# Performance work log

Measured on AMD Instinct MI355X. Metric: run time of the kernel, lower is better.

The kernel has to match this reference:

```python
import jax, jax.numpy as jnp
import numpy as np

B, L, C, H = 4, 2048, 1024, 16
D = C // H
MAX_SCALE_MUL = float(np.log(100.0))
EPS = 1e-12


def setup_inputs() -> dict:
    key = jax.random.key(0)
    ks = jax.random.split(key, 7)
    return {
        "x": jax.random.normal(ks[0], (B, L, C), dtype=jnp.float32),
        "W_qkv": jax.random.normal(ks[1], (3 * C, C), dtype=jnp.float32) * (C ** -0.5),
        "q_bias": jax.random.normal(ks[2], (C,), dtype=jnp.float32) * 0.02,
        "v_bias": jax.random.normal(ks[3], (C,), dtype=jnp.float32) * 0.02,
        "scale_mul_log": jnp.full((1, H, 1, 1), np.log(4.0), dtype=jnp.float32),
        "W_proj": jax.random.normal(ks[4], (C, C), dtype=jnp.float32) * (C ** -0.5),
        "b_proj": jax.random.normal(ks[5], (C,), dtype=jnp.float32) * 0.02,
    }


def reference(x, W_qkv, q_bias, v_bias, scale_mul_log, W_proj, b_proj):
    Bb, Ll, Cc = x.shape
    # fused QKV projection with bias = cat(q_bias, zeros, v_bias)
    bias = jnp.concatenate([q_bias, jnp.zeros_like(q_bias), v_bias])
    qkv = (x @ W_qkv.T + bias).reshape(Bb, Ll, 3, H, D)
    q, k, v = (jnp.transpose(qkv[:, :, i], (0, 2, 1, 3)) for i in range(3))  # [B,H,L,D]
    # L2-norm attention: normalize q,k; learned per-head scale on q (clamped)
    scale_mul = jnp.exp(jnp.minimum(scale_mul_log, MAX_SCALE_MUL))  # [1,H,1,1]
    q = q / jnp.maximum(jnp.linalg.norm(q, axis=-1, keepdims=True), EPS) * scale_mul
    k = k / jnp.maximum(jnp.linalg.norm(k, axis=-1, keepdims=True), EPS)
    # SDPA with scale=1 (attn_l2_norm path), no mask, no dropout (eval)
    scores = jnp.einsum("bhqd,bhkd->bhqk", q, k)
    attn = jax.nn.softmax(scores, axis=-1)
    out = jnp.einsum("bhqk,bhkd->bhqd", attn, v)
    out = jnp.transpose(out, (0, 2, 1, 3)).reshape(Bb, Ll, Cc)
    return out @ W_proj.T + b_proj
```

## Files before the change

kernel.cpp:

```cpp
#include <hip/hip_runtime.h>
#include <hip/hip_bf16.h>


typedef __attribute__((ext_vector_type(8))) short bf16x8;
typedef __attribute__((ext_vector_type(4))) float f32x4;
typedef __attribute__((ext_vector_type(16))) float f32x16;

#define MAXLOG 4.60517018598809f
#define LOG2E  1.4426950408889634f

__device__ __forceinline__ float bf2f(unsigned short u) {
    union { unsigned int i; float f; } v; v.i = ((unsigned int)u) << 16; return v.f;
}
__device__ __forceinline__ unsigned short f2bf(float f) {
    union { float f; unsigned int i; } v; v.f = f;
    unsigned int x = v.i;
    return (unsigned short)((x + 0x7FFFu + ((x >> 16) & 1u)) >> 16);
}
__device__ __forceinline__ bf16x8 pack8(const float* __restrict__ p) {
    float4 a = *(const float4*)p;
    float4 b = *(const float4*)(p + 4);
    bf16x8 r;
    r[0] = (short)f2bf(a.x); r[1] = (short)f2bf(a.y);
    r[2] = (short)f2bf(a.z); r[3] = (short)f2bf(a.w);
    r[4] = (short)f2bf(b.x); r[5] = (short)f2bf(b.y);
    r[6] = (short)f2bf(b.z); r[7] = (short)f2bf(b.w);
    return r;
}
__device__ __forceinline__ void gload_lds16(const void* g, void* l) {
    __builtin_amdgcn_global_load_lds((const __attribute__((address_space(1))) void*)g,
                                     (__attribute__((address_space(3))) void*)l, 16, 0, 0);
}

__global__ __launch_bounds__(256) void k_cast_bf16(const float* __restrict__ src,
                                                   unsigned short* __restrict__ dst, int n8) {
    int i = blockIdx.x * 256 + threadIdx.x;
    if (i < n8) *(bf16x8*)&dst[(long)i * 8] = pack8(&src[(long)i * 8]);
}

__global__ void k_build_bias(const float* __restrict__ qb, const float* __restrict__ vb,
                             float* __restrict__ bias3) {
    int i = blockIdx.x * 256 + threadIdx.x;
    if (i < 3072) {
        float v = 0.0f;
        if (i < 1024) v = qb[i];
        else if (i >= 2048) v = vb[i - 2048];
        bias3[i] = v;
    }
}

template<bool B_F32, bool OUT_F32>
__global__ __launch_bounds__(256) void k_gemm_lds(
    const unsigned short* __restrict__ A, const void* __restrict__ Bp,
    const float* __restrict__ bias, void* __restrict__ Cp, int N, int K)
{
    __shared__ unsigned short As[128 * 32];
    __shared__ unsigned short Bs[128 * 32];
    const int t = threadIdx.x, wave = t >> 6, lane = t & 63;
    const int quad = lane >> 4, l16 = lane & 15;
    const int bm = blockIdx.x * 128, bn = blockIdx.y * 128;
    const int wr = (wave >> 1) * 64, wc = (wave & 1) * 64;
    f32x4 acc[4][4] = {};

    const int srow = lane >> 2;
    const int scol = (lane & 3) * 8;
    const int c0 = wave * 2, c1 = wave * 2 + 1;
    const long ga0 = (long)(bm + c0 * 16 + srow) * K + scol;
    const long ga1 = (long)(bm + c1 * 16 + srow) * K + scol;
    const int sr = t >> 2, sc2 = (t & 3) * 8;
    const float* Bf = (const float*)Bp;
    const unsigned short* Bh = (const unsigned short*)Bp;
    const long gb0 = B_F32 ? ((long)(bn + sr) * K + sc2)      : ((long)(bn + c0 * 16 + srow) * K + scol);
    const long gb1 = B_F32 ? ((long)(bn + sr + 64) * K + sc2) : ((long)(bn + c1 * 16 + srow) * K + scol);

    for (int kt = 0; kt < K; kt += 32) {
        __syncthreads();
        gload_lds16(&A[ga0 + kt], &As[c0 * 512]);
        gload_lds16(&A[ga1 + kt], &As[c1 * 512]);
        if (B_F32) {
            *(bf16x8*)&Bs[sr * 32 + sc2]        = pack8(&Bf[gb0 + kt]);
            *(bf16x8*)&Bs[(sr + 64) * 32 + sc2] = pack8(&Bf[gb1 + kt]);
        } else {
            gload_lds16(&Bh[gb0 + kt], &Bs[c0 * 512]);
            gload_lds16(&Bh[gb1 + kt], &Bs[c1 * 512]);
        }
        __syncthreads();
        bf16x8 af[4], bfr[4];
        for (int i = 0; i < 4; ++i)
            af[i] = *(const bf16x8*)&As[(wr + i * 16 + l16) * 32 + quad * 8];
        for (int j = 0; j < 4; ++j)
            bfr[j] = *(const bf16x8*)&Bs[(wc + j * 16 + l16) * 32 + quad * 8];
        for (int i = 0; i < 4; ++i)
            for (int j = 0; j < 4; ++j)
                acc[i][j] = __builtin_amdgcn_mfma_f32_16x16x32_bf16(af[i], bfr[j], acc[i][j], 0, 0, 0);
    }
    for (int j = 0; j < 4; ++j) {
        int gn = bn + wc + j * 16 + l16;
        float bv = bias[gn];
        for (int i = 0; i < 4; ++i) {
            int gm0 = bm + wr + i * 16 + quad * 4;
            for (int r = 0; r < 4; ++r) {
                float val = acc[i][j][r] + bv;
                if (OUT_F32) ((float*)Cp)[(long)(gm0 + r) * N + gn] = val;
                else ((unsigned short*)Cp)[(long)(gm0 + r) * N + gn] = f2bf(val);
            }
        }
    }
}

__global__ __launch_bounds__(256) void k_norm_k(
    const unsigned short* __restrict__ qkv, unsigned short* __restrict__ kb)
{
    const int wid = blockIdx.x * 4 + (threadIdx.x >> 6);
    const int lane = threadIdx.x & 63;
    const int h = wid & 15, m = wid >> 4;
    const int b = m >> 11, l = m & 2047;
    float kv = bf2f(qkv[(long)m * 3072 + 1024 + h * 64 + lane]);
    float sk = kv * kv;
    for (int s = 32; s; s >>= 1) sk += __shfl_xor(sk, s, 64);
    float kn = kv / fmaxf(sqrtf(sk), 1e-12f);
    kb[((long)(b * 16 + h) * 2048 + l) * 64 + lane] = f2bf(kn);
}

__global__ __launch_bounds__(256) void k_vtrans(
    const unsigned short* __restrict__ qkv, unsigned short* __restrict__ vT)
{
    __shared__ unsigned short Vsh[64 * 72];
    const int t = threadIdx.x;
    const int bh = blockIdx.y, l0 = blockIdx.x * 64;
    const int h = bh & 15, b = bh >> 4;
    const int ll = t >> 2, d0 = (t & 3) * 16;
    long src = (long)(b * 2048 + l0 + ll) * 3072 + 2048 + h * 64 + d0;
    *(bf16x8*)&Vsh[ll * 72 + d0]     = *(const bf16x8*)&qkv[src];
    *(bf16x8*)&Vsh[ll * 72 + d0 + 8] = *(const bf16x8*)&qkv[src + 8];
    __syncthreads();
    const int d = t >> 2, ls = (t & 3) * 16;
    unsigned short tmp[16];
    for (int j = 0; j < 16; ++j) tmp[j] = Vsh[(ls + j) * 72 + d];
    long dst = (long)(bh * 64 + d) * 2048 + l0 + ls;
    *(bf16x8*)&vT[dst]     = *(bf16x8*)&tmp[0];
    *(bf16x8*)&vT[dst + 8] = *(bf16x8*)&tmp[8];
}

__global__ __launch_bounds__(256) void k_attn32(
    const unsigned short* __restrict__ qkv, const unsigned short* __restrict__ kb,
    const unsigned short* __restrict__ vT, const float* __restrict__ sml,
    unsigned short* __restrict__ attn)
{
    __shared__ unsigned short Ks[64 * 72];
    __shared__ unsigned short Vs[64 * 72];
    const int t = threadIdx.x, wave = t >> 6, lane = t & 63;
    const int m32 = lane & 31, half = lane >> 5;
    const int bh = blockIdx.y, h = bh & 15, b = bh >> 4;
    const int q0 = blockIdx.x * 128 + wave * 32;
    const float scale = __expf(fminf(sml[h], MAXLOG));
    const float c2 = scale * LOG2E;

    const int qd = m32 >> 2, lo = qd & 3;
    const int prow = ((((lo == 1) || (lo == 2)) ? (qd ^ 3) : qd) << 2) | (m32 & 3);

    bf16x8 aq[4];
    {
        long base = (long)(b * 2048 + q0 + m32) * 3072 + h * 64;
        float e[32]; float ss = 0.f;
        for (int f = 0; f < 4; ++f) {
            aq[f] = *(const bf16x8*)&qkv[base + f * 16 + half * 8];
            for (int j = 0; j < 8; ++j) { float x = bf2f((unsigned short)aq[f][j]); e[f * 8 + j] = x; ss += x * x; }
        }
        ss += __shfl_xor(ss, 32, 64);
        float rs = scale / fmaxf(sqrtf(ss), 1e-12f);
        for (int f = 0; f < 4; ++f)
            for (int j = 0; j < 8; ++j) aq[f][j] = (short)f2bf(e[f * 8 + j] * rs);
    }

    f32x16 o0 = {}, o1 = {}, lacc = {};
    bf16x8 ones; for (int i = 0; i < 8; ++i) ones[i] = (short)0x3F80;
    const int sr = t >> 2, sc = (t & 3) * 16;

    for (int kt = 0; kt < 2048; kt += 64) {
        __syncthreads();
        long ksrc = ((long)bh * 2048 + kt + sr) * 64 + sc;
        *(bf16x8*)&Ks[sr * 72 + sc]     = *(const bf16x8*)&kb[ksrc];
        *(bf16x8*)&Ks[sr * 72 + sc + 8] = *(const bf16x8*)&kb[ksrc + 8];
        long vsrc = ((long)bh * 64 + sr) * 2048 + kt + sc;
        *(bf16x8*)&Vs[sr * 72 + sc]     = *(const bf16x8*)&vT[vsrc];
        *(bf16x8*)&Vs[sr * 72 + sc + 8] = *(const bf16x8*)&vT[vsrc + 8];
        __syncthreads();

        for (int ktile = 0; ktile < 2; ++ktile) {
            f32x16 s = {};
            for (int f = 0; f < 4; ++f) {
                bf16x8 bk = *(const bf16x8*)&Ks[(ktile * 32 + prow) * 72 + f * 16 + half * 8];
                s = __builtin_amdgcn_mfma_f32_32x32x16_bf16(bk, aq[f], s, 0, 0, 0);
            }
            bf16x8 ap0, ap1;
            for (int j = 0; j < 8; ++j) {
                union { float f; unsigned int u; } cv;
                cv.f = __builtin_amdgcn_exp2f(s[j] * LOG2E - c2);
                ap0[j] = (short)(cv.u >> 16);
                cv.f = __builtin_amdgcn_exp2f(s[8 + j] * LOG2E - c2);
                ap1[j] = (short)(cv.u >> 16);
            }
            for (int c = 0; c < 2; ++c) {
                bf16x8 apc = c ? ap1 : ap0;
                bf16x8 bv0 = *(const bf16x8*)&Vs[m32 * 72        + ktile * 32 + c * 16 + half * 8];
                bf16x8 bv1 = *(const bf16x8*)&Vs[(32 + m32) * 72 + ktile * 32 + c * 16 + half * 8];
                o0   = __builtin_amdgcn_mfma_f32_32x32x16_bf16(apc, bv0, o0, 0, 0, 0);
                o1   = __builtin_amdgcn_mfma_f32_32x32x16_bf16(apc, bv1, o1, 0, 0, 0);
                lacc = __builtin_amdgcn_mfma_f32_32x32x16_bf16(apc, ones, lacc, 0, 0, 0);
            }
        }
    }
    for (int r = 0; r < 16; ++r) {
        int m = (r & 3) + 8 * (r >> 2) + 4 * half;
        float inv = 1.0f / lacc[r];
        long dst = (long)(b * 2048 + q0 + m) * 1024 + h * 64;
        attn[dst + m32]      = f2bf(o0[r] * inv);
        attn[dst + 32 + m32] = f2bf(o1[r] * inv);
    }
}

extern "C" void kernel_launch(void* const* d_in, const int* in_sizes, int n_in,
                              void* d_out, int out_size, void* d_ws, size_t ws_size,
                              hipStream_t stream) {
    const float* x    = (const float*)d_in[0];
    const float* Wqkv = (const float*)d_in[1];
    const float* qbia = (const float*)d_in[2];
    const float* vbia = (const float*)d_in[3];
    const float* sml  = (const float*)d_in[4];
    const float* Wp   = (const float*)d_in[5];
    const float* bp   = (const float*)d_in[6];

    char* ws = (char*)d_ws;
    unsigned short* qkv   = (unsigned short*)ws;
    unsigned short* kbuf  = (unsigned short*)(ws + 50331648);
    unsigned short* Wqkvb = kbuf;
    unsigned short* vT    = (unsigned short*)(ws + 67108864);
    unsigned short* xb    = vT;
    unsigned short* attn  = (unsigned short*)(ws + 83886080);
    float*          bias3 = (float*)(ws + 100663296);
    float*          out   = (float*)d_out;

    hipLaunchKernelGGL(k_cast_bf16, dim3(4096), dim3(256), 0, stream, x, xb, 1048576);
    hipLaunchKernelGGL(k_cast_bf16, dim3(1536), dim3(256), 0, stream, Wqkv, Wqkvb, 393216);
    hipLaunchKernelGGL(k_build_bias, dim3(12), dim3(256), 0, stream, qbia, vbia, bias3);
    hipLaunchKernelGGL((k_gemm_lds<false, false>), dim3(64, 24), dim3(256), 0, stream,
                       xb, (const void*)Wqkvb, bias3, (void*)qkv, 3072, 1024);
    hipLaunchKernelGGL(k_norm_k, dim3(32768), dim3(256), 0, stream, qkv, kbuf);
    hipLaunchKernelGGL(k_vtrans, dim3(32, 64), dim3(256), 0, stream, qkv, vT);
    hipLaunchKernelGGL(k_attn32, dim3(16, 64), dim3(256), 0, stream, qkv, kbuf, vT, sml, attn);
    hipLaunchKernelGGL((k_gemm_lds<true, true>), dim3(64, 8), dim3(256), 0, stream,
                       attn, (const void*)Wp, bp, (void*)out, 1024, 1024);
}
```

Measured before the change: 337.2 us.

## Double-buffer K/V tiles, compute softmax row sums in registers, pre-cast W_proj

The attention kernel now keeps two LDS buffers for K and V. It loads the next tile into registers while it computes on the current tile, which removes one barrier per step. The row sums are accumulated as scalar exp sums and combined with shuffles, replacing the extra MFMA against a ones vector. P is now converted to bf16 with round-to-nearest through byte-perm packing. Launch bounds now request 3 blocks per CU. W_proj is cast to bf16 in a separate kernel so the output projection can use a bf16 B operand. The trade-offs are more register pressure, an extra kernel launch, and reuse of the qkv workspace for Wpb after attention has finished.

```diff
diff --git a/kernel.cpp b/kernel.cpp
--- a/kernel.cpp
+++ b/kernel.cpp
@@ -16,6 +16,9 @@
     union { float f; unsigned int i; } v; v.f = f;
     unsigned int x = v.i;
     return (unsigned short)((x + 0x7FFFu + ((x >> 16) & 1u)) >> 16);
+}
+__device__ __forceinline__ unsigned fbits(float f) {
+    union { float f; unsigned u; } v; v.f = f; return v.u;
 }
 __device__ __forceinline__ bf16x8 pack8(const float* __restrict__ p) {
     float4 a = *(const float4*)p;
@@ -142,13 +145,13 @@
     *(bf16x8*)&vT[dst + 8] = *(bf16x8*)&tmp[8];
 }
 
-__global__ __launch_bounds__(256) void k_attn32(
+__global__ __launch_bounds__(256, 3) void k_attn32(
     const unsigned short* __restrict__ qkv, const unsigned short* __restrict__ kb,
     const unsigned short* __restrict__ vT, const float* __restrict__ sml,
     unsigned short* __restrict__ attn)
 {
-    __shared__ unsigned short Ks[64 * 72];
-    __shared__ unsigned short Vs[64 * 72];
+    __shared__ unsigned short Ks[2][64 * 72];
+    __shared__ unsigned short Vs[2][64 * 72];
     const int t = threadIdx.x, wave = t >> 6, lane = t & 63;
     const int m32 = lane & 31, half = lane >> 5;
     const int bh = blockIdx.y, h = bh & 15, b = bh >> 4;
@@ -173,47 +176,85 @@
             for (int j = 0; j < 8; ++j) aq[f][j] = (short)f2bf(e[f * 8 + j] * rs);
     }
 
-    f32x16 o0 = {}, o1 = {}, lacc = {};
-    bf16x8 ones; for (int i = 0; i < 8; ++i) ones[i] = (short)0x3F80;
+    f32x16 o0 = {}, o1 = {};
+    float ps0 = 0.f, ps1 = 0.f;
     const int sr = t >> 2, sc = (t & 3) * 16;
-
-    for (int kt = 0; kt < 2048; kt += 64) {
+    const long kbase = (long)bh * 2048 * 64;
+    const long vbase = (long)bh * 64 * 2048;
+
+#define LOADT(kt) \
+    kpA = *(const bf16x8*)&kb[kbase + (long)((kt) + sr) * 64 + sc];      \
+    kpB = *(const bf16x8*)&kb[kbase + (long)((kt) + sr) * 64 + sc + 8];  \
+    vpA = *(const bf16x8*)&vT[vbase + (long)sr * 2048 + (kt) + sc];      \
+    vpB = *(const bf16x8*)&vT[vbase + (long)sr * 2048 + (kt) + sc + 8];
+
+#define STORET(buf) \
+    *(bf16x8*)&Ks[buf][sr * 72 + sc]     = kpA;  \
+    *(bf16x8*)&Ks[buf][sr * 72 + sc + 8] = kpB;  \
+    *(bf16x8*)&Vs[buf][sr * 72 + sc]     = vpA;  \
+    *(bf16x8*)&Vs[buf][sr * 72 + sc + 8] = vpB;
+
+#define ATTN_STEP(KS, VS) \
+    for (int ktile = 0; ktile < 2; ++ktile) {                                             \
+        f32x16 s = {};                                                                    \
+        for (int f = 0; f < 4; ++f) {                                                     \
+            bf16x8 bk = *(const bf16x8*)&KS[(ktile * 32 + prow) * 72 + f * 16 + half * 8];\
+            s = __builtin_amdgcn_mfma_f32_32x32x16_bf16(bk, aq[f], s, 0, 0, 0);           \
+        }                                                                                 \
+        unsigned pu[16];                                                                  \
+        for (int j = 0; j < 8; ++j) {                                                     \
+            float ea = __builtin_amdgcn_exp2f(s[j] * LOG2E - c2);                         \
+            float eb = __builtin_amdgcn_exp2f(s[8 + j] * LOG2E - c2);                     \
+            ps0 += ea; ps1 += eb;                                                         \
+            pu[j] = fbits(ea) + 0x8000u; pu[8 + j] = fbits(eb) + 0x8000u;                 \
+        }                                                                                 \
+        uint4 a0u, a1u;                                                                   \
+        a0u.x = __builtin_amdgcn_perm(pu[1],  pu[0],  0x07060302u);                       \
+        a0u.y = __builtin_amdgcn_perm(pu[3],  pu[2],  0x07060302u);                       \
+        a0u.z = __builtin_amdgcn_perm(pu[5],  pu[4],  0x07060302u);                       \
+        a0u.w = __builtin_amdgcn_perm(pu[7],  pu[6],  0x07060302u);                       \
+        a1u.x = __builtin_amdgcn_perm(pu[9],  pu[8],  0x07060302u);                       \
+        a1u.y = __builtin_amdgcn_perm(pu[11], pu[10], 0x07060302u);                       \
+        a1u.z = __builtin_amdgcn_perm(pu[13], pu[12], 0x07060302u);                       \
+        a1u.w = __builtin_amdgcn_perm(pu[15], pu[14], 0x07060302u);                       \
+        bf16x8 ap0, ap1;                                                                  \
+        __builtin_memcpy(&ap0, &a0u, 16); __builtin_memcpy(&ap1, &a1u, 16);               \
+        for (int c = 0; c < 2; ++c) {                                                     \
+            bf16x8 apc = c ? ap1 : ap0;                                                   \
+            bf16x8 bv0 = *(const bf16x8*)&VS[m32 * 72        + ktile * 32 + c * 16 + half * 8]; \
+            bf16x8 bv1 = *(const bf16x8*)&VS[(32 + m32) * 72 + ktile * 32 + c * 16 + half * 8]; \
+            o0 = __builtin_amdgcn_mfma_f32_32x32x16_bf16(apc, bv0, o0, 0, 0, 0);          \
+            o1 = __builtin_amdgcn_mfma_f32_32x32x16_bf16(apc, bv1, o1, 0, 0, 0);          \
+        }                                                                                 \
+    }
+
+    bf16x8 kpA, kpB, vpA, vpB;
+    LOADT(0)
+    STORET(0)
+    __syncthreads();
+
+    for (int kt = 0; kt < 2048; kt += 128) {
+        LOADT(kt + 64)
+        ATTN_STEP(Ks[0], Vs[0])
+        STORET(1)
         __syncthreads();
-        long ksrc = ((long)bh * 2048 + kt + sr) * 64 + sc;
-        *(bf16x8*)&Ks[sr * 72 + sc]     = *(const bf16x8*)&kb[ksrc];
-        *(bf16x8*)&Ks[sr * 72 + sc + 8] = *(const bf16x8*)&kb[ksrc + 8];
-        long vsrc = ((long)bh * 64 + sr) * 2048 + kt + sc;
-        *(bf16x8*)&Vs[sr * 72 + sc]     = *(const bf16x8*)&vT[vsrc];
-        *(bf16x8*)&Vs[sr * 72 + sc + 8] = *(const bf16x8*)&vT[vsrc + 8];
-        __syncthreads();
-
-        for (int ktile = 0; ktile < 2; ++ktile) {
-            f32x16 s = {};
-            for (int f = 0; f < 4; ++f) {
-                bf16x8 bk = *(const bf16x8*)&Ks[(ktile * 32 + prow) * 72 + f * 16 + half * 8];
-                s = __builtin_amdgcn_mfma_f32_32x32x16_bf16(bk, aq[f], s, 0, 0, 0);
-            }
-            bf16x8 ap0, ap1;
-            for (int j = 0; j < 8; ++j) {
-                union { float f; unsigned int u; } cv;
-                cv.f = __builtin_amdgcn_exp2f(s[j] * LOG2E - c2);
-                ap0[j] = (short)(cv.u >> 16);
-                cv.f = __builtin_amdgcn_exp2f(s[8 + j] * LOG2E - c2);
-                ap1[j] = (short)(cv.u >> 16);
-            }
-            for (int c = 0; c < 2; ++c) {
-                bf16x8 apc = c ? ap1 : ap0;
-                bf16x8 bv0 = *(const bf16x8*)&Vs[m32 * 72        + ktile * 32 + c * 16 + half * 8];
-                bf16x8 bv1 = *(const bf16x8*)&Vs[(32 + m32) * 72 + ktile * 32 + c * 16 + half * 8];
-                o0   = __builtin_amdgcn_mfma_f32_32x32x16_bf16(apc, bv0, o0, 0, 0, 0);
-                o1   = __builtin_amdgcn_mfma_f32_32x32x16_bf16(apc, bv1, o1, 0, 0, 0);
-                lacc = __builtin_amdgcn_mfma_f32_32x32x16_bf16(apc, ones, lacc, 0, 0, 0);
-            }
-        }
-    }
+        const bool more = (kt + 128) < 2048;
+        if (more) { LOADT(kt + 128) }
+        ATTN_STEP(Ks[1], Vs[1])
+        if (more) {
+            STORET(0)
+            __syncthreads();
+        }
+    }
+#undef LOADT
+#undef STORET
+#undef ATTN_STEP
+
+    float fl = ps0 + ps1;
+    fl += __shfl_xor(fl, 32, 64);
     for (int r = 0; r < 16; ++r) {
         int m = (r & 3) + 8 * (r >> 2) + 4 * half;
-        float inv = 1.0f / lacc[r];
+        float inv = 1.0f / __shfl(fl, m, 64);
         long dst = (long)(b * 2048 + q0 + m) * 1024 + h * 64;
         attn[dst + m32]      = f2bf(o0[r] * inv);
         attn[dst + 32 + m32] = f2bf(o1[r] * inv);
@@ -233,6 +274,7 @@
 
     char* ws = (char*)d_ws;
     unsigned short* qkv   = (unsigned short*)ws;
+    unsigned short* Wpb   = (unsigned short*)ws;
     unsigned short* kbuf  = (unsigned short*)(ws + 50331648);
     unsigned short* Wqkvb = kbuf;
     unsigned short* vT    = (unsigned short*)(ws + 67108864);
@@ -249,6 +291,7 @@
     hipLaunchKernelGGL(k_norm_k, dim3(32768), dim3(256), 0, stream, qkv, kbuf);
     hipLaunchKernelGGL(k_vtrans, dim3(32, 64), dim3(256), 0, stream, qkv, vT);
     hipLaunchKernelGGL(k_attn32, dim3(16, 64), dim3(256), 0, stream, qkv, kbuf, vT, sml, attn);
-    hipLaunchKernelGGL((k_gemm_lds<true, true>), dim3(64, 8), dim3(256), 0, stream,
-                       attn, (const void*)Wp, bp, (void*)out, 1024, 1024);
-}
+    hipLaunchKernelGGL(k_cast_bf16, dim3(512), dim3(256), 0, stream, Wp, Wpb, 131072);
+    hipLaunchKernelGGL((k_gemm_lds<false, true>), dim3(64, 8), dim3(256), 0, stream,
+                       attn, (const void*)Wpb, bp, (void*)out, 1024, 1024);
+}
```

Measured after the change: 321.8 us. 4.6% less time.
